# Performance work log

Hardware: AMD Instinct MI355X
Metric: run time of the kernel (lower is better)

Reference implementation:

```python
import jax, jax.numpy as jnp
import numpy as np
import math

BS, N_CTX, WIDTH, HEADS = 4, 2048, 1024, 16
INIT_SCALE = 0.02

def setup_inputs() -> dict:
    key = jax.random.key(0)
    ks = jax.random.split(key, 5)
    x = jax.random.normal(ks[0], (BS, N_CTX, WIDTH), dtype=jnp.float32)
    w_qkv = jax.random.normal(ks[1], (WIDTH, 3 * WIDTH), dtype=jnp.float32) * INIT_SCALE
    b_qkv = jnp.zeros((3 * WIDTH,), dtype=jnp.float32)
    w_proj = jax.random.normal(ks[2], (WIDTH, WIDTH), dtype=jnp.float32) * INIT_SCALE
    b_proj = jnp.zeros((WIDTH,), dtype=jnp.float32)
    return {"x": x, "w_qkv": w_qkv, "b_qkv": b_qkv, "w_proj": w_proj, "b_proj": b_proj}

def reference(x, w_qkv, b_qkv, w_proj, b_proj):
    bs, n_ctx, width = x.shape
    heads = HEADS
    qkv = x @ w_qkv + b_qkv  # [b, t, 3*width]
    attn_ch = (3 * width) // heads // 3  # head dim
    scale = 1.0 / math.sqrt(math.sqrt(attn_ch))
    qkv = qkv.reshape(bs, n_ctx, heads, 3 * attn_ch)
    q, k, v = jnp.split(qkv, 3, axis=-1)  # each [b, s, h, c]
    weight = jnp.einsum('bthc,bshc->bhts', q * scale, k * scale)
    weight = jax.nn.softmax(weight.astype(jnp.float32), axis=-1).astype(weight.dtype)
    out = jnp.einsum('bhts,bshc->bthc', weight, v).reshape(bs, n_ctx, width)
    return out @ w_proj + b_proj
```

## Files before the change

kernel.cpp:

```cpp
#include <hip/hip_runtime.h>
#include <stdint.h>

#define MM   8192
#define KK   1024
#define NQKV 3072
#define TT   2048
#define HH   16
#define DD   64

typedef __attribute__((ext_vector_type(8))) short bf16x8;
typedef __attribute__((ext_vector_type(4))) short short4v;
typedef __attribute__((ext_vector_type(4))) float f32x4;
typedef __attribute__((ext_vector_type(16))) float f32x16;
typedef __attribute__((ext_vector_type(4))) unsigned int u32x4;

#define MFMA16(a,b,c)  __builtin_amdgcn_mfma_f32_16x16x32_bf16(a,b,c,0,0,0)
#define MFMA32(a,b,c)  __builtin_amdgcn_mfma_f32_32x32x16_bf16(a,b,c,0,0,0)

static __device__ __forceinline__ short f2bf(float f) {
    uint32_t u = __float_as_uint(f);
    uint32_t r = (u + 0x7fffu + ((u >> 16) & 1u)) >> 16;
    return (short)r;
}

static __device__ __forceinline__ float fexp2(float x) {
    float r;
    asm("v_exp_f32 %0, %1" : "=v"(r) : "v"(x));
    return r;
}

static __device__ __forceinline__ uint32_t cvtpk(float a, float b) {
    uint32_t r;
    asm("v_cvt_pk_bf16_f32 %0, %1, %2" : "=v"(r) : "v"(a), "v"(b));
    return r;
}

static __device__ __forceinline__ void plswap(uint32_t& x, uint32_t& y) {
    asm("v_permlane32_swap_b32 %0, %1" : "+v"(x), "+v"(y));
}

static __device__ __forceinline__ float tsum16(const f32x16& p) {
    float a0 = p[0] + p[8],  a1 = p[1] + p[9];
    float a2 = p[2] + p[10], a3 = p[3] + p[11];
    float a4 = p[4] + p[12], a5 = p[5] + p[13];
    float a6 = p[6] + p[14], a7 = p[7] + p[15];
    float b0 = a0 + a4, b1 = a1 + a5, b2 = a2 + a6, b3 = a3 + a7;
    return (b0 + b2) + (b1 + b3);
}

__global__ __launch_bounds__(256) void convert_x(const float* __restrict__ x,
                                                 short* __restrict__ xb, int n) {
    int i = (blockIdx.x * 256 + threadIdx.x) * 4;
    if (i >= n) return;
    float4 v = *(const float4*)(x + i);
    short4v o;
    o[0] = f2bf(v.x); o[1] = f2bf(v.y); o[2] = f2bf(v.z); o[3] = f2bf(v.w);
    *(short4v*)(xb + i) = o;
}

__global__ __launch_bounds__(256) void transpose_w(const float* __restrict__ Wf,
                                                   short* __restrict__ Wt, int K, int N) {
    __shared__ float tile[32][33];
    const int n0 = blockIdx.x * 32, k0 = blockIdx.y * 32;
    const int tx = threadIdx.x & 31, ty = threadIdx.x >> 5;
#pragma unroll
    for (int i = 0; i < 4; ++i) {
        int k = ty + i * 8;
        tile[k][tx] = Wf[(size_t)(k0 + k) * N + n0 + tx];
    }
    __syncthreads();
#pragma unroll
    for (int i = 0; i < 4; ++i) {
        int n = ty + i * 8;
        Wt[(size_t)(n0 + n) * K + k0 + tx] = f2bf(tile[tx][n]);
    }
}

template <int N, bool F32OUT>
__global__ __launch_bounds__(256) void gemm_bt(const short* __restrict__ A,
                                               const short* __restrict__ Bt,
                                               const float* __restrict__ bias,
                                               void* __restrict__ Cout, int K) {
    __shared__ short As[128 * 72];
    __shared__ short Bs[128 * 72];
    const int tid = threadIdx.x, lane = tid & 63, wave = tid >> 6;
    const int l15 = lane & 15, lg = lane >> 4;
    const int wm = wave >> 1, wn = wave & 1;
    const int m0 = blockIdx.y * 128, n0 = blockIdx.x * 128;

    f32x4 zero = {0.f, 0.f, 0.f, 0.f};
    f32x4 acc[4][4];
#pragma unroll
    for (int i = 0; i < 4; ++i)
#pragma unroll
        for (int j = 0; j < 4; ++j) acc[i][j] = zero;

    const int sr = tid >> 3, sc = (tid & 7) * 8;

    for (int kt = 0; kt < K; kt += 64) {
#pragma unroll
        for (int p = 0; p < 4; ++p) {
            int row = sr + p * 32;
            *(bf16x8*)(&As[row * 72 + sc]) = *(const bf16x8*)(A + (size_t)(m0 + row) * K + kt + sc);
            *(bf16x8*)(&Bs[row * 72 + sc]) = *(const bf16x8*)(Bt + (size_t)(n0 + row) * K + kt + sc);
        }
        __syncthreads();
#pragma unroll
        for (int ks = 0; ks < 2; ++ks) {
            bf16x8 af[4], bfr[4];
#pragma unroll
            for (int i = 0; i < 4; ++i)
                af[i] = *(const bf16x8*)(&As[(wm * 64 + i * 16 + l15) * 72 + ks * 32 + lg * 8]);
#pragma unroll
            for (int j = 0; j < 4; ++j)
                bfr[j] = *(const bf16x8*)(&Bs[(wn * 64 + j * 16 + l15) * 72 + ks * 32 + lg * 8]);
#pragma unroll
            for (int i = 0; i < 4; ++i)
#pragma unroll
                for (int j = 0; j < 4; ++j)
                    acc[i][j] = MFMA16(af[i], bfr[j], acc[i][j]);
        }
        __syncthreads();
    }
#pragma unroll
    for (int j = 0; j < 4; ++j) {
        int col = n0 + wn * 64 + j * 16 + l15;
        float bv = bias[col];
#pragma unroll
        for (int i = 0; i < 4; ++i) {
            int row = m0 + wm * 64 + i * 16 + lg * 4;
#pragma unroll
            for (int r = 0; r < 4; ++r) {
                float v = acc[i][j][r] + bv;
                if (F32OUT)
                    ((float*)Cout)[(size_t)(row + r) * N + col] = v;
                else
                    ((short*)Cout)[(size_t)(row + r) * N + col] = f2bf(v);
            }
        }
    }
}

__global__ __launch_bounds__(256) void repack_kv(const short* __restrict__ QKV,
                                                 short* __restrict__ Kf,
                                                 short* __restrict__ Vf) {
    __shared__ short Kl[64 * 72];
    __shared__ short Vl[64 * 72];
    const int t = blockIdx.x, bh = blockIdx.y;
    const int b = bh >> 4, h = bh & 15;
    const int tid = threadIdx.x;
    const int r = tid >> 3, c = (tid & 7) * 8;
    const short* kvbase = QKV + (size_t)(b * TT + t * 64) * NQKV + h * 192;
#pragma unroll
    for (int p = 0; p < 2; ++p) {
        int row = r + p * 32;
        *(bf16x8*)(&Kl[row * 72 + c]) = *(const bf16x8*)(kvbase + (size_t)row * NQKV + 64 + c);
        *(bf16x8*)(&Vl[row * 72 + c]) = *(const bf16x8*)(kvbase + (size_t)row * NQKV + 128 + c);
    }
    __syncthreads();
    short* kfb = Kf + ((size_t)bh * 32 + t) * 4096;
    short* vfb = Vf + ((size_t)bh * 32 + t) * 4096;
#pragma unroll
    for (int p = 0; p < 2; ++p) {
        int q = tid + p * 256;
        int lane = q & 63, dc = (q >> 6) & 3, half = q >> 8;
        int l31 = lane & 31, hi = lane >> 5;
        bf16x8 kv = *(const bf16x8*)(&Kl[(half * 32 + l31) * 72 + hi * 8 + dc * 16]);
        *(bf16x8*)(kfb + q * 8) = kv;
        bf16x8 vv;
#pragma unroll
        for (int j = 0; j < 8; ++j)
            vv[j] = Vl[(hi * 8 + dc * 16 + j) * 72 + half * 32 + l31];
        *(bf16x8*)(vfb + q * 8) = vv;
    }
}

static __device__ __forceinline__ void attn_tile(
    const bf16x8 (&kc0)[4], const bf16x8 (&kc1)[4],
    bf16x8 (&kn0)[4], bf16x8 (&kn1)[4],
    const bf16x8 (&qf)[4],
    const short* __restrict__ kfb, const short* __restrict__ vfb,
    int t, int lane8,
    f32x16& o0, f32x16& o1, float& ls) {

    int nxt = t + 1; nxt = (nxt < TT / 64) ? nxt : 0;
    const short* np = kfb + (size_t)nxt * 4096 + lane8;
#pragma unroll
    for (int dc = 0; dc < 4; ++dc) kn0[dc] = *(const bf16x8*)(np + dc * 512);
#pragma unroll
    for (int dc = 0; dc < 4; ++dc) kn1[dc] = *(const bf16x8*)(np + 2048 + dc * 512);

    const short* vp = vfb + (size_t)t * 4096 + lane8;
    bf16x8 vf0[4], vf1[4];
#pragma unroll
    for (int ks = 0; ks < 4; ++ks) vf0[ks] = *(const bf16x8*)(vp + ks * 512);
#pragma unroll
    for (int ks = 0; ks < 4; ++ks) vf1[ks] = *(const bf16x8*)(vp + 2048 + ks * 512);

    f32x16 s0, s1;
#pragma unroll
    for (int i = 0; i < 16; ++i) { s0[i] = 0.f; s1[i] = 0.f; }
#pragma unroll
    for (int dc = 0; dc < 4; ++dc) s0 = MFMA32(kc0[dc], qf[dc], s0);
#pragma unroll
    for (int dc = 0; dc < 4; ++dc) s1 = MFMA32(kc1[dc], qf[dc], s1);

#pragma unroll
    for (int i = 0; i < 16; ++i) s0[i] = fexp2(s0[i]);
#pragma unroll
    for (int i = 0; i < 16; ++i) s1[i] = fexp2(s1[i]);

    float rs = tsum16(s0) + tsum16(s1);
    rs += __shfl_xor(rs, 32);
    ls += rs;

    uint32_t a0 = cvtpk(s0[0], s0[1]),   a1 = cvtpk(s0[2], s0[3]);
    uint32_t b0 = cvtpk(s0[4], s0[5]),   b1 = cvtpk(s0[6], s0[7]);
    plswap(a0, b0); plswap(a1, b1);
    uint32_t c0 = cvtpk(s0[8], s0[9]),   c1 = cvtpk(s0[10], s0[11]);
    uint32_t d0 = cvtpk(s0[12], s0[13]), d1 = cvtpk(s0[14], s0[15]);
    plswap(c0, d0); plswap(c1, d1);
    uint32_t e0 = cvtpk(s1[0], s1[1]),   e1 = cvtpk(s1[2], s1[3]);
    uint32_t f0 = cvtpk(s1[4], s1[5]),   f1 = cvtpk(s1[6], s1[7]);
    plswap(e0, f0); plswap(e1, f1);
    uint32_t g0 = cvtpk(s1[8], s1[9]),   g1 = cvtpk(s1[10], s1[11]);
    uint32_t h0 = cvtpk(s1[12], s1[13]), h1 = cvtpk(s1[14], s1[15]);
    plswap(g0, h0); plswap(g1, h1);
    u32x4 w0 = {a0, a1, b0, b1};
    u32x4 w1 = {c0, c1, d0, d1};
    u32x4 w2 = {e0, e1, f0, f1};
    u32x4 w3 = {g0, g1, h0, h1};
    bf16x8 pa0 = __builtin_bit_cast(bf16x8, w0);
    bf16x8 pa1 = __builtin_bit_cast(bf16x8, w1);
    bf16x8 pa2 = __builtin_bit_cast(bf16x8, w2);
    bf16x8 pa3 = __builtin_bit_cast(bf16x8, w3);

    o0 = MFMA32(vf0[0], pa0, o0);
    o0 = MFMA32(vf0[1], pa1, o0);
    o0 = MFMA32(vf0[2], pa2, o0);
    o0 = MFMA32(vf0[3], pa3, o0);
    o1 = MFMA32(vf1[0], pa0, o1);
    o1 = MFMA32(vf1[1], pa1, o1);
    o1 = MFMA32(vf1[2], pa2, o1);
    o1 = MFMA32(vf1[3], pa3, o1);
}

__global__ __launch_bounds__(128) void attn_fwd(const short* __restrict__ QKV,
                                                const short* __restrict__ Kf,
                                                const short* __restrict__ Vf,
                                                short* __restrict__ Out) {
    const int qb = blockIdx.x, bh = blockIdx.y;
    const int b = bh >> 4, h = bh & 15;
    const int lane = threadIdx.x & 63, wave = threadIdx.x >> 6;
    const int l31 = lane & 31, hi = lane >> 5;
    const int q0 = qb * 64 + wave * 32;
    const int lane8 = lane * 8;

    const short* qptr = QKV + (size_t)(b * TT + q0 + l31) * NQKV + h * 192 + hi * 8;
    bf16x8 qf[4];
#pragma unroll
    for (int dc = 0; dc < 4; ++dc) qf[dc] = *(const bf16x8*)(qptr + dc * 16);

    const float cc = 0.18033688011112042f;
    {
        short* qs = (short*)qf;
#pragma unroll
        for (int i = 0; i < 32; ++i) {
            float v = __uint_as_float(((uint32_t)(uint16_t)qs[i]) << 16) * cc;
            qs[i] = f2bf(v);
        }
    }

    const short* kfb = Kf + (size_t)bh * 32 * 4096;
    const short* vfb = Vf + (size_t)bh * 32 * 4096;

    f32x16 o0, o1;
#pragma unroll
    for (int i = 0; i < 16; ++i) { o0[i] = 0.f; o1[i] = 0.f; }
    float ls = 0.f;

    bf16x8 kA0[4], kA1[4], kB0[4], kB1[4];
#pragma unroll
    for (int dc = 0; dc < 4; ++dc) kA0[dc] = *(const bf16x8*)(kfb + dc * 512 + lane8);
#pragma unroll
    for (int dc = 0; dc < 4; ++dc) kA1[dc] = *(const bf16x8*)(kfb + 2048 + dc * 512 + lane8);

    for (int t = 0; t < TT / 64; t += 2) {
        attn_tile(kA0, kA1, kB0, kB1, qf, kfb, vfb, t,     lane8, o0, o1, ls);
        attn_tile(kB0, kB1, kA0, kA1, qf, kfb, vfb, t + 1, lane8, o0, o1, ls);
    }

    float inv = 1.0f / ls;
    short* orow = Out + (size_t)(b * TT + q0 + l31) * (HH * DD) + h * DD;
#pragma unroll
    for (int g = 0; g < 4; ++g) {
        short4v v0, v1;
#pragma unroll
        for (int r = 0; r < 4; ++r) {
            v0[r] = f2bf(o0[g * 4 + r] * inv);
            v1[r] = f2bf(o1[g * 4 + r] * inv);
        }
        *(short4v*)(orow + g * 8 + hi * 4) = v0;
        *(short4v*)(orow + 32 + g * 8 + hi * 4) = v1;
    }
}

extern "C" void kernel_launch(void* const* d_in, const int* in_sizes, int n_in,
                              void* d_out, int out_size, void* d_ws, size_t ws_size,
                              hipStream_t stream) {
    const float* x      = (const float*)d_in[0];
    const float* w_qkv  = (const float*)d_in[1];
    const float* b_qkv  = (const float*)d_in[2];
    const float* w_proj = (const float*)d_in[3];
    const float* b_proj = (const float*)d_in[4];
    float* out = (float*)d_out;

    char* ws = (char*)d_ws;
    short* xb     = (short*)(ws);
    short* vf     = (short*)(ws);
    short* wqkvt  = (short*)(ws + 16777216);
    short* wprojt = (short*)(ws + 23068672);
    short* qkv    = (short*)(ws + 25165824);
    short* kf     = (short*)(ws + 75497472);
    short* ao     = (short*)(ws + 92274688);

    convert_x<<<8192, 256, 0, stream>>>(x, xb, MM * KK);
    transpose_w<<<dim3(NQKV / 32, KK / 32), 256, 0, stream>>>(w_qkv, wqkvt, KK, NQKV);
    transpose_w<<<dim3(KK / 32, KK / 32), 256, 0, stream>>>(w_proj, wprojt, KK, KK);
    gemm_bt<NQKV, false><<<dim3(NQKV / 128, MM / 128), 256, 0, stream>>>(xb, wqkvt, b_qkv, qkv, KK);
    repack_kv<<<dim3(TT / 64, 64), 256, 0, stream>>>(qkv, kf, vf);
    attn_fwd<<<dim3(TT / 64, 64), 128, 0, stream>>>(qkv, kf, vf, ao);
    gemm_bt<KK, true><<<dim3(KK / 128, MM / 128), 256, 0, stream>>>(ao, wprojt, b_proj, out, KK);
}
```

Measured before the change: 212.9 us.

## Fuse K/V repack into QKV GEMM epilogue and add XCD-aware block swizzle

The QKV GEMM epilogue now writes Q to a compact per-head buffer and scatters K and V directly into the MFMA-friendly fragment layouts, removing the separate repack_kv kernel and its extra read and write of the QKV tensor. GEMM and attention launches become 1D grids remapped with an XCD swizzle, so blocks that share data land on the same XCD's L2. The scattered scalar 2-byte stores in the epilogue are poorly coalesced, which may cost more GEMM time than the launch and traffic it saves.

Result: faster. 205.2 us (median of 2 runs) (-3.6%).

```diff
diff --git a/kernel.cpp b/kernel.cpp
--- a/kernel.cpp
+++ b/kernel.cpp
@@ -46,6 +46,13 @@
     float a6 = p[6] + p[14], a7 = p[7] + p[15];
     float b0 = a0 + a4, b1 = a1 + a5, b2 = a2 + a6, b3 = a3 + a7;
     return (b0 + b2) + (b1 + b3);
+}
+
+static __device__ __forceinline__ int xcd_swz(int orig, int nwg) {
+    int q = nwg >> 3, r = nwg & 7;
+    int xcd = orig & 7, idx = orig >> 3;
+    return (xcd < r) ? (xcd * (q + 1) + idx)
+                     : (r * (q + 1) + (xcd - r) * q + idx);
 }
 
 __global__ __launch_bounds__(256) void convert_x(const float* __restrict__ x,
@@ -76,17 +83,22 @@
     }
 }
 
-template <int N, bool F32OUT>
+template <int N, int EPI>
 __global__ __launch_bounds__(256) void gemm_bt(const short* __restrict__ A,
                                                const short* __restrict__ Bt,
                                                const float* __restrict__ bias,
-                                               void* __restrict__ Cout, int K) {
+                                               void* __restrict__ Cout,
+                                               short* __restrict__ Kf,
+                                               short* __restrict__ Vf, int K) {
     __shared__ short As[128 * 72];
     __shared__ short Bs[128 * 72];
+    const int nwg = (N / 128) * (MM / 128);
+    const int wg = xcd_swz(blockIdx.x, nwg);
+    const int bx = wg % (N / 128), by = wg / (N / 128);
     const int tid = threadIdx.x, lane = tid & 63, wave = tid >> 6;
     const int l15 = lane & 15, lg = lane >> 4;
     const int wm = wave >> 1, wn = wave & 1;
-    const int m0 = blockIdx.y * 128, n0 = blockIdx.x * 128;
+    const int m0 = by * 128, n0 = bx * 128;
 
     f32x4 zero = {0.f, 0.f, 0.f, 0.f};
     f32x4 acc[4][4];
@@ -122,56 +134,45 @@
         }
         __syncthreads();
     }
+
 #pragma unroll
     for (int j = 0; j < 4; ++j) {
         int col = n0 + wn * 64 + j * 16 + l15;
         float bv = bias[col];
-#pragma unroll
-        for (int i = 0; i < 4; ++i) {
-            int row = m0 + wm * 64 + i * 16 + lg * 4;
-#pragma unroll
-            for (int r = 0; r < 4; ++r) {
-                float v = acc[i][j][r] + bv;
-                if (F32OUT)
-                    ((float*)Cout)[(size_t)(row + r) * N + col] = v;
-                else
-                    ((short*)Cout)[(size_t)(row + r) * N + col] = f2bf(v);
+        if (EPI == 0) {
+#pragma unroll
+            for (int i = 0; i < 4; ++i) {
+                int row = m0 + wm * 64 + i * 16 + lg * 4;
+#pragma unroll
+                for (int r = 0; r < 4; ++r)
+                    ((float*)Cout)[(size_t)(row + r) * N + col] = acc[i][j][r] + bv;
             }
-        }
-    }
-}
-
-__global__ __launch_bounds__(256) void repack_kv(const short* __restrict__ QKV,
-                                                 short* __restrict__ Kf,
-                                                 short* __restrict__ Vf) {
-    __shared__ short Kl[64 * 72];
-    __shared__ short Vl[64 * 72];
-    const int t = blockIdx.x, bh = blockIdx.y;
-    const int b = bh >> 4, h = bh & 15;
-    const int tid = threadIdx.x;
-    const int r = tid >> 3, c = (tid & 7) * 8;
-    const short* kvbase = QKV + (size_t)(b * TT + t * 64) * NQKV + h * 192;
-#pragma unroll
-    for (int p = 0; p < 2; ++p) {
-        int row = r + p * 32;
-        *(bf16x8*)(&Kl[row * 72 + c]) = *(const bf16x8*)(kvbase + (size_t)row * NQKV + 64 + c);
-        *(bf16x8*)(&Vl[row * 72 + c]) = *(const bf16x8*)(kvbase + (size_t)row * NQKV + 128 + c);
-    }
-    __syncthreads();
-    short* kfb = Kf + ((size_t)bh * 32 + t) * 4096;
-    short* vfb = Vf + ((size_t)bh * 32 + t) * 4096;
-#pragma unroll
-    for (int p = 0; p < 2; ++p) {
-        int q = tid + p * 256;
-        int lane = q & 63, dc = (q >> 6) & 3, half = q >> 8;
-        int l31 = lane & 31, hi = lane >> 5;
-        bf16x8 kv = *(const bf16x8*)(&Kl[(half * 32 + l31) * 72 + hi * 8 + dc * 16]);
-        *(bf16x8*)(kfb + q * 8) = kv;
-        bf16x8 vv;
-#pragma unroll
-        for (int j = 0; j < 8; ++j)
-            vv[j] = Vl[(hi * 8 + dc * 16 + j) * 72 + half * 32 + l31];
-        *(bf16x8*)(vfb + q * 8) = vv;
+        } else {
+            int h = col / 192, seg = col - h * 192;
+#pragma unroll
+            for (int i = 0; i < 4; ++i) {
+#pragma unroll
+                for (int r = 0; r < 4; ++r) {
+                    int row = m0 + wm * 64 + i * 16 + lg * 4 + r;
+                    short v = f2bf(acc[i][j][r] + bv);
+                    if (seg < 64) {
+                        ((short*)Cout)[(size_t)row * (HH * DD) + h * DD + seg] = v;
+                    } else {
+                        int key = row & (TT - 1), b = row >> 11;
+                        size_t base = ((size_t)(b * HH + h) * 32 + (key >> 6)) * 4096;
+                        if (seg < 128) {
+                            int d = seg - 64;
+                            Kf[base + ((key >> 5) & 1) * 2048 + (d >> 4) * 512
+                               + ((key & 31) + 32 * ((d >> 3) & 1)) * 8 + (d & 7)] = v;
+                        } else {
+                            int d = seg - 128;
+                            Vf[base + (d >> 5) * 2048 + ((key >> 4) & 3) * 512
+                               + ((d & 31) + 32 * ((key >> 3) & 1)) * 8 + (key & 7)] = v;
+                        }
+                    }
+                }
+            }
+        }
     }
 }
 
@@ -245,18 +246,19 @@
     o1 = MFMA32(vf1[3], pa3, o1);
 }
 
-__global__ __launch_bounds__(128) void attn_fwd(const short* __restrict__ QKV,
+__global__ __launch_bounds__(128) void attn_fwd(const short* __restrict__ Qt,
                                                 const short* __restrict__ Kf,
                                                 const short* __restrict__ Vf,
                                                 short* __restrict__ Out) {
-    const int qb = blockIdx.x, bh = blockIdx.y;
+    const int wg = xcd_swz(blockIdx.x, (TT / 64) * 64);
+    const int qb = wg & 31, bh = wg >> 5;
     const int b = bh >> 4, h = bh & 15;
     const int lane = threadIdx.x & 63, wave = threadIdx.x >> 6;
     const int l31 = lane & 31, hi = lane >> 5;
     const int q0 = qb * 64 + wave * 32;
     const int lane8 = lane * 8;
 
-    const short* qptr = QKV + (size_t)(b * TT + q0 + l31) * NQKV + h * 192 + hi * 8;
+    const short* qptr = Qt + (size_t)(b * TT + q0 + l31) * (HH * DD) + h * DD + hi * 8;
     bf16x8 qf[4];
 #pragma unroll
     for (int dc = 0; dc < 4; ++dc) qf[dc] = *(const bf16x8*)(qptr + dc * 16);
@@ -317,18 +319,19 @@
 
     char* ws = (char*)d_ws;
     short* xb     = (short*)(ws);
-    short* vf     = (short*)(ws);
     short* wqkvt  = (short*)(ws + 16777216);
     short* wprojt = (short*)(ws + 23068672);
-    short* qkv    = (short*)(ws + 25165824);
-    short* kf     = (short*)(ws + 75497472);
-    short* ao     = (short*)(ws + 92274688);
+    short* qt     = (short*)(ws + 25165824);
+    short* kf     = (short*)(ws + 41943040);
+    short* vf     = (short*)(ws + 58720256);
+    short* ao     = (short*)(ws + 75497472);
 
     convert_x<<<8192, 256, 0, stream>>>(x, xb, MM * KK);
     transpose_w<<<dim3(NQKV / 32, KK / 32), 256, 0, stream>>>(w_qkv, wqkvt, KK, NQKV);
     transpose_w<<<dim3(KK / 32, KK / 32), 256, 0, stream>>>(w_proj, wprojt, KK, KK);
-    gemm_bt<NQKV, false><<<dim3(NQKV / 128, MM / 128), 256, 0, stream>>>(xb, wqkvt, b_qkv, qkv, KK);
-    repack_kv<<<dim3(TT / 64, 64), 256, 0, stream>>>(qkv, kf, vf);
-    attn_fwd<<<dim3(TT / 64, 64), 128, 0, stream>>>(qkv, kf, vf, ao);
-    gemm_bt<KK, true><<<dim3(KK / 128, MM / 128), 256, 0, stream>>>(ao, wprojt, b_proj, out, KK);
-}
+    gemm_bt<NQKV, 1><<<(NQKV / 128) * (MM / 128), 256, 0, stream>>>(
+        xb, wqkvt, b_qkv, qt, kf, vf, KK);
+    attn_fwd<<<(TT / 64) * 64, 128, 0, stream>>>(qt, kf, vf, ao);
+    gemm_bt<KK, 0><<<(KK / 128) * (MM / 128), 256, 0, stream>>>(
+        ao, wprojt, b_proj, out, nullptr, nullptr, KK);
+}
```
